# Kernel tuning notes

Hardware: AMD Instinct MI355X
Metric: run time of the kernel (lower is better)

The kernel has to match this reference:

```python
import jax, jax.numpy as jnp
from jax import lax
import numpy as np

B, T, K = 128, 256, 600


def setup_inputs() -> dict:
    key = jax.random.key(0)
    k1, k2, k3, k4 = jax.random.split(key, 4)
    potentials = jax.random.normal(k1, (B, T, K), dtype=jnp.float32)
    transitions = jax.random.normal(k2, (K, K), dtype=jnp.float32) * 0.1
    tags = jax.random.randint(k3, (B, T), 0, K, dtype=jnp.int32)
    seq_len = jax.random.randint(k4, (B,), T // 2, T + 1, dtype=jnp.int32)
    return {"potentials": potentials, "transitions": transitions,
            "tags": tags, "seq_len": seq_len}


def _sequence_score(potentials, transitions, tags, mask):
    # unary (emission) scores: sum_t potentials[b, t, tags[b, t]] over valid t
    emit = jnp.take_along_axis(potentials, tags[..., None], axis=-1)[..., 0]  # [B,T]
    unary = jnp.sum(emit * mask, axis=1)
    # binary (transition) scores for valid consecutive pairs
    trans = transitions[tags[:, :-1], tags[:, 1:]]  # [B,T-1]
    binary = jnp.sum(trans * mask[:, 1:], axis=1)
    return unary + binary


def _log_norm(potentials, transitions, mask):
    # forward algorithm over time via scan; alpha: [B,K]
    def step(alpha, inp):
        emit_t, mask_t = inp  # [B,K], [B]
        scores = alpha[:, :, None] + transitions[None]      # [B,K,K]
        new = jax.nn.logsumexp(scores, axis=1) + emit_t     # [B,K]
        alpha = jnp.where(mask_t[:, None], new, alpha)
        return alpha, None

    alpha0 = potentials[:, 0]
    xs = (jnp.swapaxes(potentials[:, 1:], 0, 1),
          jnp.swapaxes(mask[:, 1:] > 0, 0, 1))
    alpha, _ = lax.scan(step, alpha0, xs)
    return jax.nn.logsumexp(alpha, axis=-1)  # [B]


def _viterbi(potentials, transitions, mask):
    idk = jnp.arange(K, dtype=jnp.int32)

    def step(alpha, inp):
        emit_t, mask_t = inp
        scores = alpha[:, :, None] + transitions[None]   # [B,K,K]
        bp = jnp.argmax(scores, axis=1).astype(jnp.int32)  # [B,K]
        new = jnp.max(scores, axis=1) + emit_t
        alpha = jnp.where(mask_t[:, None], new, alpha)
        bp = jnp.where(mask_t[:, None], bp, idk[None, :])  # identity past seq end
        return alpha, bp

    alpha0 = potentials[:, 0]
    xs = (jnp.swapaxes(potentials[:, 1:], 0, 1),
          jnp.swapaxes(mask[:, 1:] > 0, 0, 1))
    alpha, bps = lax.scan(step, alpha0, xs)  # bps: [T-1,B,K]
    last = jnp.argmax(alpha, axis=-1).astype(jnp.int32)  # [B]

    def back(tag, bp):
        prev = jnp.take_along_axis(bp, tag[:, None], axis=1)[:, 0]
        return prev, prev

    _, prevs = lax.scan(back, last, bps, reverse=True)  # [T-1,B]
    seq = jnp.concatenate([prevs, last[None]], axis=0)  # [T,B]
    seq = jnp.swapaxes(seq, 0, 1)                       # [B,T]
    return seq * mask.astype(jnp.int32)


def reference(potentials, transitions, tags, seq_len):
    mask = (jnp.arange(T)[None, :] < seq_len[:, None]).astype(potentials.dtype)  # [B,T]
    score = _sequence_score(potentials, transitions, tags, mask)
    log_norm = _log_norm(potentials, transitions, mask)
    log_likelihood = score - log_norm            # [B]
    crf_loss = -jnp.mean(log_likelihood)         # scalar, as in train_step
    decode_sequence = _viterbi(potentials, transitions, mask)  # [B,T]
    return crf_loss, decode_sequence
```

## Files before the change

kernel.cpp:

```cpp
#include <hip/hip_runtime.h>
#include <stdint.h>

#define CRF_B 128
#define CRF_T 256
#define CRF_K 600
#define FWD_NT 640
#define NWAVE 10
#define QW 152
#define QG 92
#define QSTR (QW - QG)
#define ESC 60.0f
#define INV7620 (1.0f/7620.0f)

#if __has_builtin(__builtin_amdgcn_sdot4)
#define DOT4(a,b,c) __builtin_amdgcn_sdot4((int)(a),(int)(b),(int)(c),false)
#else
__device__ __forceinline__ int DOT4(uint32_t a, uint32_t b, int c) {
    c += (int)(int8_t)(a)       * (int)(int8_t)(b);
    c += (int)(int8_t)(a >> 8)  * (int)(int8_t)(b >> 8);
    c += (int)(int8_t)(a >> 16) * (int)(int8_t)(b >> 16);
    c += (int)(int8_t)(a >> 24) * (int)(int8_t)(b >> 24);
    return c;
}
#endif

__device__ __forceinline__ uint32_t fmono(float x) {
    uint32_t k = __float_as_uint(x);
    return (k & 0x80000000u) ? ~k : (k | 0x80000000u);
}
__device__ __forceinline__ float funmono(uint32_t k) {
    return __uint_as_float((k & 0x80000000u) ? (k ^ 0x80000000u) : ~k);
}

__global__ __launch_bounds__(256) void prepE_kernel(const float* __restrict__ trans,
                                                    uint32_t* __restrict__ EqT)
{
    int idx = blockIdx.x * 256 + threadIdx.x;
    if (idx < QW * CRF_K) {
        int q = idx / CRF_K, j = idx % CRF_K;
        uint32_t w = 0;
        #pragma unroll
        for (int k = 0; k < 4; ++k) {
            int i = 4 * q + k;
            int b = 0;
            if (i < CRF_K) {
                b = __float2int_rn(ESC * __expf(trans[i * CRF_K + j]));
                b = min(127, max(0, b));
            }
            w |= ((uint32_t)(b & 0xff)) << (8 * k);
        }
        EqT[idx] = w;
    }
}

__global__ __launch_bounds__(64) void prep2_kernel(const float* __restrict__ trans,
                                                   float* __restrict__ rowmax,
                                                   float* __restrict__ rowmin)
{
    int r = blockIdx.x;
    int lane = threadIdx.x;
    float mx = -INFINITY, mn = INFINITY;
    for (int j = lane; j < CRF_K; j += 64) {
        float v = trans[r * CRF_K + j];
        mx = fmaxf(mx, v);
        mn = fminf(mn, v);
    }
    for (int o = 32; o; o >>= 1) {
        mx = fmaxf(mx, __shfl_down(mx, o));
        mn = fminf(mn, __shfl_down(mn, o));
    }
    if (lane == 0) { rowmax[r] = mx; rowmin[r] = mn; }
}

__global__ __launch_bounds__(64) void score_kernel(const float* __restrict__ pot,
                                                   const float* __restrict__ trans,
                                                   const int* __restrict__ tags,
                                                   const int* __restrict__ seq_len,
                                                   float* __restrict__ scoreArr)
{
    int b = blockIdx.x;
    int lane = threadIdx.x;
    int L = seq_len[b];
    float s = 0.f;
    for (int t = lane; t < CRF_T; t += 64) {
        if (t < L) {
            int tg = tags[b * CRF_T + t];
            s += pot[((size_t)b * CRF_T + t) * CRF_K + tg];
            if (t >= 1) {
                int tp = tags[b * CRF_T + t - 1];
                s += trans[tp * CRF_K + tg];
            }
        }
    }
    for (int o = 32; o; o >>= 1) s += __shfl_down(s, o);
    if (lane == 0) scoreArr[b] = s;
}

#define CHUNK(APTR, EPTR, CH) { \
    uint4 a  = *(const uint4*)((APTR) + 4 * (CH)); \
    uint4 e0 = *(const uint4*)((EPTR) + (size_t)(4 * (CH) + 0) * CRF_K); \
    uint4 e1 = *(const uint4*)((EPTR) + (size_t)(4 * (CH) + 1) * CRF_K); \
    uint4 e2 = *(const uint4*)((EPTR) + (size_t)(4 * (CH) + 2) * CRF_K); \
    uint4 e3 = *(const uint4*)((EPTR) + (size_t)(4 * (CH) + 3) * CRF_K); \
    S0 = DOT4(a.x, e0.x, S0); S1 = DOT4(a.x, e0.y, S1); S2 = DOT4(a.x, e0.z, S2); S3 = DOT4(a.x, e0.w, S3); \
    S0 = DOT4(a.y, e1.x, S0); S1 = DOT4(a.y, e1.y, S1); S2 = DOT4(a.y, e1.z, S2); S3 = DOT4(a.y, e1.w, S3); \
    S0 = DOT4(a.z, e2.x, S0); S1 = DOT4(a.z, e2.y, S1); S2 = DOT4(a.z, e2.z, S2); S3 = DOT4(a.z, e2.w, S3); \
    S0 = DOT4(a.w, e3.x, S0); S1 = DOT4(a.w, e3.y, S1); S2 = DOT4(a.w, e3.z, S2); S3 = DOT4(a.w, e3.w, S3); }

__global__ __launch_bounds__(FWD_NT, 2) void fwd_kernel(
    const float* __restrict__ pot,
    const float* __restrict__ trans,
    const uint32_t* __restrict__ EqT,
    const float* __restrict__ rowmax,
    const float* __restrict__ rowmin,
    const int* __restrict__ seq_len,
    uint16_t* __restrict__ bp,
    float* __restrict__ lognormArr,
    int* __restrict__ lastArr)
{
    extern __shared__ uint32_t eLds[];
    const int bid = blockIdx.x;
    const int tid = threadIdx.x;
    const int lane = tid & 63, wid = tid >> 6;
    const bool act = tid < CRF_K;

    __shared__ __align__(16) float sAv[2][CRF_K];
    __shared__ int sCand[FWD_NT];
    __shared__ int sRedI[NWAVE];
    __shared__ __align__(16) uint32_t sAq[2][QW];
    __shared__ float sRedA[NWAVE];
    __shared__ unsigned vSlot[2];
    __shared__ unsigned lSlot[2];
    __shared__ float sB0f;
    __shared__ int sRedC[NWAVE];

    if (bid < CRF_B) {
        const int b = bid;
        const int L = seq_len[b];
        const float* pb = pot + (size_t)b * CRF_T * CRF_K;
        float rmx = act ? rowmax[tid] : 0.f;
        float rmn = act ? rowmin[tid] : 0.f;
        if (act) sAv[0][tid] = pb[tid];
        if (tid == 0) { vSlot[0] = 0u; vSlot[1] = 0u; }
        int cur = 0;
        __syncthreads();

        for (int t = 1; t < L; ++t) {
            float a_own = act ? sAv[cur][tid] : -INFINITY;
            float li = act ? a_own + rmn : -INFINITY;
            for (int o = 32; o; o >>= 1) li = fmaxf(li, __shfl_down(li, o));
            if (lane == 0) atomicMax(&vSlot[t & 1], fmono(li));
            __syncthreads();
            const float LB = funmono(vSlot[t & 1]);
            if (tid == 0) vSlot[(t + 1) & 1] = 0u;
            bool flag = act && (a_own + rmx >= LB);
            uint64_t mask = __ballot(flag);
            if (flag) sCand[(wid << 6) + __popcll(mask & ((1ull << lane) - 1ull))] = tid;
            if (lane == 0) sRedI[wid] = __popcll(mask);
            __syncthreads();
            float emitv = act ? pb[(size_t)t * CRF_K + tid] : 0.f;
            if (act) {
                float v = -INFINITY; int ix = 0;
                #pragma unroll 2
                for (int w = 0; w < NWAVE; ++w) {
                    const int cw = sRedI[w];
                    const int base = w << 6;
                    for (int k0 = 0; k0 < cw; k0 += 4) {
                        #pragma unroll
                        for (int u = 0; u < 4; ++u) {
                            int kk = k0 + u;
                            int i = sCand[base + ((kk < cw) ? kk : 0)];
                            float cnd = sAv[cur][i] + trans[i * CRF_K + tid];
                            if (cnd > v) { v = cnd; ix = i; }
                        }
                    }
                }
                bp[((size_t)b * (CRF_T - 1) + (t - 1)) * CRF_K + tid] = (uint16_t)ix;
                sAv[cur ^ 1][tid] = v + emitv;
            }
            cur ^= 1;
        }

        float mv = act ? sAv[cur][tid] : -INFINITY;
        float y = mv;
        for (int o = 32; o; o >>= 1) y = fmaxf(y, __shfl_down(y, o));
        if (lane == 0) sRedA[wid] = y;
        __syncthreads();
        if (tid == 0) { float m = sRedA[0]; for (int w = 1; w < NWAVE; ++w) m = fmaxf(m, sRedA[w]); sB0f = m; }
        __syncthreads();
        float vmax = sB0f;
        int cand = (act && mv == vmax) ? tid : 0x7fffffff;
        for (int o = 32; o; o >>= 1) cand = min(cand, __shfl_down(cand, o));
        if (lane == 0) sRedC[wid] = cand;
        __syncthreads();
        if (tid == 0) {
            int mi = sRedC[0];
            for (int w = 1; w < NWAVE; ++w) mi = min(mi, sRedC[w]);
            lastArr[b] = mi;
        }
    } else {
        const int b = bid - CRF_B;
        const int L = seq_len[b];
        const float* pb = pot + (size_t)b * CRF_T * CRF_K;
        const bool cact = tid < CRF_K / 4;
        const int j0 = 4 * tid;

        for (int w = tid; w < QSTR * CRF_K; w += FWD_NT)
            eLds[w] = EqT[(size_t)QG * CRF_K + w];

        float4 p0 = cact ? *(const float4*)(pb + j0)
                         : make_float4(-INFINITY, -INFINITY, -INFINITY, -INFINITY);
        {
            float y = fmaxf(fmaxf(p0.x, p0.y), fmaxf(p0.z, p0.w));
            for (int o = 32; o; o >>= 1) y = fmaxf(y, __shfl_down(y, o));
            if (lane == 0) sRedA[wid] = y;
            __syncthreads();
            if (tid == 0) { float m = sRedA[0]; for (int w = 1; w < NWAVE; ++w) m = fmaxf(m, sRedA[w]); sB0f = m; }
            __syncthreads();
        }
        float m0 = sB0f;
        float ls = m0, lsf = m0;
        float afin = 0.f;
        if (cact) {
            uint32_t w = 0;
            w |= (uint32_t)(__float2int_rn(127.0f * __expf(p0.x - m0)) & 0xff);
            w |= (uint32_t)(__float2int_rn(127.0f * __expf(p0.y - m0)) & 0xff) << 8;
            w |= (uint32_t)(__float2int_rn(127.0f * __expf(p0.z - m0)) & 0xff) << 16;
            w |= (uint32_t)(__float2int_rn(127.0f * __expf(p0.w - m0)) & 0xff) << 24;
            sAq[0][tid] = w;
        }
        if (tid >= 636) {
            sAq[0][150 + (tid & 1)] = 0u;
            sAq[1][150 + (tid & 1)] = 0u;
        }
        if (tid == 0) { lSlot[0] = 0u; lSlot[1] = 0u; }
        int cur = 0;
        __syncthreads();

        for (int t = 1; t < L; ++t) {
            float na0 = 0.f, na1 = 0.f, na2 = 0.f, na3 = 0.f;
            if (cact) {
                int S0 = 0, S1 = 0, S2 = 0, S3 = 0;
                const uint32_t* eg = EqT + j0;
                #pragma unroll 4
                for (int ch = 0; ch < QG / 4; ++ch) CHUNK(&sAq[cur][0], eg, ch)
                const uint32_t* el = eLds + j0;
                #pragma unroll 4
                for (int ch = 0; ch < QSTR / 4; ++ch) CHUNK(&sAq[cur][QG], el, ch)
                float4 em = *(const float4*)(pb + (size_t)t * CRF_K + j0);
                na0 = (float)S0 * INV7620 * __expf(em.x);
                na1 = (float)S1 * INV7620 * __expf(em.y);
                na2 = (float)S2 * INV7620 * __expf(em.z);
                na3 = (float)S3 * INV7620 * __expf(em.w);
            }
            float mx = fmaxf(fmaxf(na0, na1), fmaxf(na2, na3));
            for (int o = 32; o; o >>= 1) mx = fmaxf(mx, __shfl_down(mx, o));
            if (lane == 0) atomicMax(&lSlot[t & 1], __float_as_uint(mx));
            __syncthreads();
            float m = __uint_as_float(lSlot[t & 1]);
            if (tid == 0) lSlot[(t + 1) & 1] = 0u;
            if (t == L - 1) { afin = na0 + na1 + na2 + na3; lsf = ls; }
            ls += __logf(m);
            if (cact) {
                float s = 127.0f / m;
                uint32_t w = 0;
                w |= (uint32_t)(__float2int_rn(na0 * s) & 0xff);
                w |= (uint32_t)(__float2int_rn(na1 * s) & 0xff) << 8;
                w |= (uint32_t)(__float2int_rn(na2 * s) & 0xff) << 16;
                w |= (uint32_t)(__float2int_rn(na3 * s) & 0xff) << 24;
                sAq[cur ^ 1][tid] = w;
            }
            __syncthreads();
            cur ^= 1;
        }

        float a0s = afin;
        for (int o = 32; o; o >>= 1) a0s += __shfl_down(a0s, o);
        if (lane == 0) sRedA[wid] = a0s;
        __syncthreads();
        if (tid == 0) {
            float S = 0.f;
            for (int w = 0; w < NWAVE; ++w) S += sRedA[w];
            lognormArr[b] = lsf + __logf(S);
        }
    }
}

__global__ __launch_bounds__(64) void backtrace_kernel(const uint16_t* __restrict__ bp,
                                                       const int* __restrict__ seq_len,
                                                       const int* __restrict__ lastArr,
                                                       float* __restrict__ out)
{
    int r = blockIdx.x * 64 + threadIdx.x;
    if (r >= CRF_B) return;
    int L = seq_len[r];
    float* o = out + 1 + (size_t)r * CRF_T;
    int tag = lastArr[r];
    for (int t = CRF_T - 1; t >= L; --t) o[t] = 0.f;
    o[L - 1] = (float)tag;
    for (int t = L - 2; t >= 0; --t) {
        tag = bp[((size_t)r * (CRF_T - 1) + t) * CRF_K + tag];
        o[t] = (float)tag;
    }
}

__global__ __launch_bounds__(128) void loss_kernel(const float* __restrict__ scoreArr,
                                                   const float* __restrict__ lognormArr,
                                                   float* __restrict__ out)
{
    int tid = threadIdx.x;
    float x = scoreArr[tid] - lognormArr[tid];
    for (int o = 32; o; o >>= 1) x += __shfl_down(x, o);
    __shared__ float r2[2];
    if ((tid & 63) == 0) r2[tid >> 6] = x;
    __syncthreads();
    if (tid == 0) out[0] = -(r2[0] + r2[1]) / (float)CRF_B;
}

extern "C" void kernel_launch(void* const* d_in, const int* in_sizes, int n_in,
                              void* d_out, int out_size, void* d_ws, size_t ws_size,
                              hipStream_t stream)
{
    const float* pot     = (const float*)d_in[0];
    const float* trans   = (const float*)d_in[1];
    const int*   tags    = (const int*)d_in[2];
    const int*   seq_len = (const int*)d_in[3];
    float* out = (float*)d_out;

    char* ws = (char*)d_ws;
    const size_t bpBytes  = (size_t)CRF_B * (CRF_T - 1) * CRF_K * 2;
    const size_t eqBytes  = (size_t)QW * CRF_K * 4;
    uint16_t* bp     = (uint16_t*)ws;
    uint32_t* EqT    = (uint32_t*)(ws + bpBytes);
    float*    rowmax = (float*)(ws + bpBytes + eqBytes);
    float*    rowmin = rowmax + CRF_K;
    float* scoreArr   = rowmin + CRF_K;
    float* lognormArr = scoreArr + CRF_B;
    int*   lastArr    = (int*)(lognormArr + CRF_B);

    prepE_kernel<<<(QW * CRF_K + 255) / 256, 256, 0, stream>>>(trans, EqT);
    prep2_kernel<<<CRF_K, 64, 0, stream>>>(trans, rowmax, rowmin);
    score_kernel<<<CRF_B, 64, 0, stream>>>(pot, trans, tags, seq_len, scoreArr);
    fwd_kernel<<<2 * CRF_B, FWD_NT, QSTR * CRF_K * 4, stream>>>(
        pot, trans, EqT, rowmax, rowmin, seq_len, bp, lognormArr, lastArr);
    backtrace_kernel<<<(CRF_B + 63) / 64, 64, 0, stream>>>(bp, seq_len, lastArr, out);
    loss_kernel<<<1, 128, 0, stream>>>(scoreArr, lognormArr, out);
}
```

Measured before the change: 1.982 ms.

## Split forward int8 dot products across four thread groups with LDS partial-sum reduction

The log-normalizer blocks previously used only 150 of 640 threads for the int8 dot-product matvec each timestep. The k-dimension is now split into four slices, one per 150-thread group, and each group writes partial sums to shared memory. One group then reduces them. Emission loads are prefetched one step ahead, the global/LDS split moves to 96/56 rows, and the Viterbi candidate loop is unrolled by 8. This adds an extra barrier and a 9.6KB LDS buffer per step, which may reduce occupancy.

Result: slower. 2.217 ms (+11.8%).

```diff
diff --git a/kernel.cpp b/kernel.cpp
--- a/kernel.cpp
+++ b/kernel.cpp
@@ -7,8 +7,8 @@
 #define FWD_NT 640
 #define NWAVE 10
 #define QW 152
-#define QG 92
-#define QSTR (QW - QG)
+#define QG 96
+#define QL (QW - QG)
 #define ESC 60.0f
 #define INV7620 (1.0f/7620.0f)
 
@@ -96,16 +96,41 @@
     if (lane == 0) scoreArr[b] = s;
 }
 
-#define CHUNK(APTR, EPTR, CH) { \
-    uint4 a  = *(const uint4*)((APTR) + 4 * (CH)); \
-    uint4 e0 = *(const uint4*)((EPTR) + (size_t)(4 * (CH) + 0) * CRF_K); \
-    uint4 e1 = *(const uint4*)((EPTR) + (size_t)(4 * (CH) + 1) * CRF_K); \
-    uint4 e2 = *(const uint4*)((EPTR) + (size_t)(4 * (CH) + 2) * CRF_K); \
-    uint4 e3 = *(const uint4*)((EPTR) + (size_t)(4 * (CH) + 3) * CRF_K); \
-    S0 = DOT4(a.x, e0.x, S0); S1 = DOT4(a.x, e0.y, S1); S2 = DOT4(a.x, e0.z, S2); S3 = DOT4(a.x, e0.w, S3); \
-    S0 = DOT4(a.y, e1.x, S0); S1 = DOT4(a.y, e1.y, S1); S2 = DOT4(a.y, e1.z, S2); S3 = DOT4(a.y, e1.w, S3); \
-    S0 = DOT4(a.z, e2.x, S0); S1 = DOT4(a.z, e2.y, S1); S2 = DOT4(a.z, e2.z, S2); S3 = DOT4(a.z, e2.w, S3); \
-    S0 = DOT4(a.w, e3.x, S0); S1 = DOT4(a.w, e3.y, S1); S2 = DOT4(a.w, e3.z, S2); S3 = DOT4(a.w, e3.w, S3); }
+template<int CH0, int NG_, int NL_>
+__device__ __forceinline__ void dot_range(const uint32_t* __restrict__ egj,
+                                          const uint32_t* __restrict__ elj,
+                                          const uint32_t* __restrict__ aq,
+                                          int& S0, int& S1, int& S2, int& S3)
+{
+    #pragma unroll
+    for (int k = 0; k < NG_; ++k) {
+        const int CH = CH0 + k;
+        uint4 a = *(const uint4*)(aq + 4 * CH);
+        const uint32_t* p = egj + (size_t)(4 * CH) * CRF_K;
+        uint4 e0 = *(const uint4*)(p);
+        uint4 e1 = *(const uint4*)(p + CRF_K);
+        uint4 e2 = *(const uint4*)(p + 2 * CRF_K);
+        uint4 e3 = *(const uint4*)(p + 3 * CRF_K);
+        S0 = DOT4(a.x, e0.x, S0); S1 = DOT4(a.x, e0.y, S1); S2 = DOT4(a.x, e0.z, S2); S3 = DOT4(a.x, e0.w, S3);
+        S0 = DOT4(a.y, e1.x, S0); S1 = DOT4(a.y, e1.y, S1); S2 = DOT4(a.y, e1.z, S2); S3 = DOT4(a.y, e1.w, S3);
+        S0 = DOT4(a.z, e2.x, S0); S1 = DOT4(a.z, e2.y, S1); S2 = DOT4(a.z, e2.z, S2); S3 = DOT4(a.z, e2.w, S3);
+        S0 = DOT4(a.w, e3.x, S0); S1 = DOT4(a.w, e3.y, S1); S2 = DOT4(a.w, e3.z, S2); S3 = DOT4(a.w, e3.w, S3);
+    }
+    #pragma unroll
+    for (int k = 0; k < NL_; ++k) {
+        const int CH = CH0 + NG_ + k;
+        uint4 a = *(const uint4*)(aq + 4 * CH);
+        const uint32_t* p = elj + (size_t)(4 * CH - QG) * CRF_K;
+        uint4 e0 = *(const uint4*)(p);
+        uint4 e1 = *(const uint4*)(p + CRF_K);
+        uint4 e2 = *(const uint4*)(p + 2 * CRF_K);
+        uint4 e3 = *(const uint4*)(p + 3 * CRF_K);
+        S0 = DOT4(a.x, e0.x, S0); S1 = DOT4(a.x, e0.y, S1); S2 = DOT4(a.x, e0.z, S2); S3 = DOT4(a.x, e0.w, S3);
+        S0 = DOT4(a.y, e1.x, S0); S1 = DOT4(a.y, e1.y, S1); S2 = DOT4(a.y, e1.z, S2); S3 = DOT4(a.y, e1.w, S3);
+        S0 = DOT4(a.z, e2.x, S0); S1 = DOT4(a.z, e2.y, S1); S2 = DOT4(a.z, e2.z, S2); S3 = DOT4(a.z, e2.w, S3);
+        S0 = DOT4(a.w, e3.x, S0); S1 = DOT4(a.w, e3.y, S1); S2 = DOT4(a.w, e3.z, S2); S3 = DOT4(a.w, e3.w, S3);
+    }
+}
 
 __global__ __launch_bounds__(FWD_NT, 2) void fwd_kernel(
     const float* __restrict__ pot,
@@ -128,6 +153,7 @@
     __shared__ int sCand[FWD_NT];
     __shared__ int sRedI[NWAVE];
     __shared__ __align__(16) uint32_t sAq[2][QW];
+    __shared__ __align__(16) int sP[4][CRF_K];
     __shared__ float sRedA[NWAVE];
     __shared__ unsigned vSlot[2];
     __shared__ unsigned lSlot[2];
@@ -165,9 +191,9 @@
                 for (int w = 0; w < NWAVE; ++w) {
                     const int cw = sRedI[w];
                     const int base = w << 6;
-                    for (int k0 = 0; k0 < cw; k0 += 4) {
+                    for (int k0 = 0; k0 < cw; k0 += 8) {
                         #pragma unroll
-                        for (int u = 0; u < 4; ++u) {
+                        for (int u = 0; u < 8; ++u) {
                             int kk = k0 + u;
                             int i = sCand[base + ((kk < cw) ? kk : 0)];
                             float cnd = sAv[cur][i] + trans[i * CRF_K + tid];
@@ -202,14 +228,16 @@
         const int b = bid - CRF_B;
         const int L = seq_len[b];
         const float* pb = pot + (size_t)b * CRF_T * CRF_K;
-        const bool cact = tid < CRF_K / 4;
-        const int j0 = 4 * tid;
-
-        for (int w = tid; w < QSTR * CRF_K; w += FWD_NT)
+        const int g  = tid / 150;
+        const int c  = tid % 150;
+        const int jd = 4 * c;
+        const int jc = 4 * tid;
+
+        for (int w = tid; w < QL * CRF_K; w += FWD_NT)
             eLds[w] = EqT[(size_t)QG * CRF_K + w];
 
-        float4 p0 = cact ? *(const float4*)(pb + j0)
-                         : make_float4(-INFINITY, -INFINITY, -INFINITY, -INFINITY);
+        float4 p0 = (tid < 150) ? *(const float4*)(pb + jc)
+                                : make_float4(-INFINITY, -INFINITY, -INFINITY, -INFINITY);
         {
             float y = fmaxf(fmaxf(p0.x, p0.y), fmaxf(p0.z, p0.w));
             for (int o = 32; o; o >>= 1) y = fmaxf(y, __shfl_down(y, o));
@@ -221,7 +249,7 @@
         float m0 = sB0f;
         float ls = m0, lsf = m0;
         float afin = 0.f;
-        if (cact) {
+        if (tid < 150) {
             uint32_t w = 0;
             w |= (uint32_t)(__float2int_rn(127.0f * __expf(p0.x - m0)) & 0xff);
             w |= (uint32_t)(__float2int_rn(127.0f * __expf(p0.y - m0)) & 0xff) << 8;
@@ -235,33 +263,51 @@
         }
         if (tid == 0) { lSlot[0] = 0u; lSlot[1] = 0u; }
         int cur = 0;
+        float4 emc = make_float4(0.f, 0.f, 0.f, 0.f), emn;
+        if (tid < 150) emc = *(const float4*)(pb + (size_t)1 * CRF_K + jc);
         __syncthreads();
 
         for (int t = 1; t < L; ++t) {
+            if (tid < CRF_K) {
+                int S0 = 0, S1 = 0, S2 = 0, S3 = 0;
+                const uint32_t* egj = EqT + jd;
+                const uint32_t* elj = eLds + jd;
+                const uint32_t* aq  = &sAq[cur][0];
+                if      (g == 0) dot_range< 0, 10, 0>(egj, elj, aq, S0, S1, S2, S3);
+                else if (g == 1) dot_range<10, 10, 0>(egj, elj, aq, S0, S1, S2, S3);
+                else if (g == 2) dot_range<20,  4, 6>(egj, elj, aq, S0, S1, S2, S3);
+                else             dot_range<30,  0, 8>(egj, elj, aq, S0, S1, S2, S3);
+                *(int4*)&sP[g][jd] = make_int4(S0, S1, S2, S3);
+            }
+            __syncthreads();
             float na0 = 0.f, na1 = 0.f, na2 = 0.f, na3 = 0.f;
-            if (cact) {
-                int S0 = 0, S1 = 0, S2 = 0, S3 = 0;
-                const uint32_t* eg = EqT + j0;
-                #pragma unroll 4
-                for (int ch = 0; ch < QG / 4; ++ch) CHUNK(&sAq[cur][0], eg, ch)
-                const uint32_t* el = eLds + j0;
-                #pragma unroll 4
-                for (int ch = 0; ch < QSTR / 4; ++ch) CHUNK(&sAq[cur][QG], el, ch)
-                float4 em = *(const float4*)(pb + (size_t)t * CRF_K + j0);
-                na0 = (float)S0 * INV7620 * __expf(em.x);
-                na1 = (float)S1 * INV7620 * __expf(em.y);
-                na2 = (float)S2 * INV7620 * __expf(em.z);
-                na3 = (float)S3 * INV7620 * __expf(em.w);
+            if (tid < 150) {
+                int4 q0 = *(const int4*)&sP[0][jc];
+                int4 q1 = *(const int4*)&sP[1][jc];
+                int4 q2 = *(const int4*)&sP[2][jc];
+                int4 q3 = *(const int4*)&sP[3][jc];
+                int S0 = (q0.x + q1.x) + (q2.x + q3.x);
+                int S1 = (q0.y + q1.y) + (q2.y + q3.y);
+                int S2 = (q0.z + q1.z) + (q2.z + q3.z);
+                int S3 = (q0.w + q1.w) + (q2.w + q3.w);
+                na0 = (float)S0 * INV7620 * __expf(emc.x);
+                na1 = (float)S1 * INV7620 * __expf(emc.y);
+                na2 = (float)S2 * INV7620 * __expf(emc.z);
+                na3 = (float)S3 * INV7620 * __expf(emc.w);
             }
             float mx = fmaxf(fmaxf(na0, na1), fmaxf(na2, na3));
             for (int o = 32; o; o >>= 1) mx = fmaxf(mx, __shfl_down(mx, o));
             if (lane == 0) atomicMax(&lSlot[t & 1], __float_as_uint(mx));
+            if (tid < 150) {
+                int tn = (t + 1 < L) ? t + 1 : t;
+                emn = *(const float4*)(pb + (size_t)tn * CRF_K + jc);
+            }
             __syncthreads();
             float m = __uint_as_float(lSlot[t & 1]);
             if (tid == 0) lSlot[(t + 1) & 1] = 0u;
             if (t == L - 1) { afin = na0 + na1 + na2 + na3; lsf = ls; }
             ls += __logf(m);
-            if (cact) {
+            if (tid < 150) {
                 float s = 127.0f / m;
                 uint32_t w = 0;
                 w |= (uint32_t)(__float2int_rn(na0 * s) & 0xff);
@@ -269,6 +315,7 @@
                 w |= (uint32_t)(__float2int_rn(na2 * s) & 0xff) << 16;
                 w |= (uint32_t)(__float2int_rn(na3 * s) & 0xff) << 24;
                 sAq[cur ^ 1][tid] = w;
+                emc = emn;
             }
             __syncthreads();
             cur ^= 1;
@@ -341,7 +388,7 @@
     prepE_kernel<<<(QW * CRF_K + 255) / 256, 256, 0, stream>>>(trans, EqT);
     prep2_kernel<<<CRF_K, 64, 0, stream>>>(trans, rowmax, rowmin);
     score_kernel<<<CRF_B, 64, 0, stream>>>(pot, trans, tags, seq_len, scoreArr);
-    fwd_kernel<<<2 * CRF_B, FWD_NT, QSTR * CRF_K * 4, stream>>>(
+    fwd_kernel<<<2 * CRF_B, FWD_NT, QL * CRF_K * 4, stream>>>(
         pot, trans, EqT, rowmax, rowmin, seq_len, bp, lognormArr, lastArr);
     backtrace_kernel<<<(CRF_B + 63) / 64, 64, 0, stream>>>(bp, seq_len, lastArr, out);
     loss_kernel<<<1, 128, 0, stream>>>(scoreArr, lognormArr, out);
```
